# Kernel tuning notes

Measured on AMD Instinct MI355X. Metric: run time of the kernel, lower is better.

The kernel has to match this reference:

```python
import jax, jax.numpy as jnp
import numpy as np

B, D, FD, HW, NH, NC = 8, 384, 256, 64, 8, 4
NP = HW * HW
HD = D // NH


def _ln(x, g, b, eps=1e-5):
    m = jnp.mean(x, -1, keepdims=True)
    v = jnp.mean((x - m) ** 2, -1, keepdims=True)
    return (x - m) / jnp.sqrt(v + eps) * g + b


def _grn(x, g, b, eps=1e-6):
    # x: [B, D, H, W]; global L2 norm per channel over spatial dims
    gx = jnp.sqrt(jnp.sum(x * x, axis=(-2, -1), keepdims=True))  # [B,D,1,1]
    nx = gx / (jnp.mean(gx, axis=-3, keepdims=True) + eps)
    return (1.0 + g[:, None, None]) * (x * nx) + b[:, None, None] + x


def _adaln(x, film, W, bW, g, b):
    gb = film @ W.T + bW                       # [B, 2D]
    gamma, beta = jnp.split(gb, 2, axis=-1)
    return _grn(x, g, b) * (1.0 + gamma)[:, :, None, None] + beta[:, :, None, None]


def setup_inputs() -> dict:
    ks = jax.random.split(jax.random.key(0), 24)
    n = lambda k, s: jax.random.normal(k, s, jnp.float32)
    w = lambda k, o, i: n(k, (o, i)) * 0.02
    return {
        "image": n(ks[0], (B, D, HW, HW)),
        "film_vector": n(ks[1], (B, FD)),
        "perm": jax.random.permutation(ks[2], NP).astype(jnp.int32),
        "Wq": w(ks[3], D, D), "bq": jnp.zeros(D),
        "Wk": w(ks[4], D, D), "bk": jnp.zeros(D),
        "Wv": w(ks[5], D, D), "bv": jnp.zeros(D),
        "Wo": w(ks[6], D, D), "bo": jnp.zeros(D),
        "lnq_g": jnp.ones(D), "lnq_b": jnp.zeros(D),
        "lnk_g": jnp.ones(D), "lnk_b": jnp.zeros(D),
        "ada1_W": n(ks[7], (2 * D, FD)) * 0.001, "ada1_b": jnp.zeros(2 * D),
        "grn1_g": jnp.zeros(D), "grn1_b": jnp.zeros(D),
        "ada2_W": n(ks[8], (2 * D, FD)) * 0.001, "ada2_b": jnp.zeros(2 * D),
        "grn2_g": jnp.zeros(D), "grn2_b": jnp.zeros(D),
        "conv1_W": w(ks[9], 4 * D, D), "conv1_b": jnp.zeros(4 * D),
        "conv2_W": w(ks[10], D, 4 * D), "conv2_b": jnp.zeros(D),
        "cloud_scalar": jnp.ones(D),
        "ffn_scalar": jnp.ones(D),
        "final_scalar": jnp.ones(D) * 0.1,
        "num_clouds": NC,
    }


def reference(image, film_vector, perm, Wq, bq, Wk, bk, Wv, bv, Wo, bo,
              lnq_g, lnq_b, lnk_g, lnk_b, ada1_W, ada1_b, grn1_g, grn1_b,
              ada2_W, ada2_b, grn2_g, grn2_b, conv1_W, conv1_b, conv2_W, conv2_b,
              cloud_scalar, ffn_scalar, final_scalar, num_clouds):
    b, d, h, w = image.shape
    tp = h * w
    gs = tp // num_clouds

    # ---- cloud attention branch ----
    x = _adaln(image, film_vector, ada1_W, ada1_b, grn1_g, grn1_b)
    x_sh = x.reshape(b, d, tp)[:, :, perm]                       # shuffled pixels
    xg = x_sh.transpose(0, 2, 1).reshape(b * num_clouds, gs, d)  # [b*nc, gs, d]

    q = _ln(xg @ Wq.T + bq, lnq_g, lnq_b)
    k = _ln(xg @ Wk.T + bk, lnk_g, lnk_b)
    v = (xg @ Wv.T + bv).reshape(-1, gs, NH, HD)
    q = jax.nn.elu(q.reshape(-1, gs, NH, HD)) + 1.0
    k = jax.nn.elu(k.reshape(-1, gs, NH, HD)) + 1.0

    kv = jnp.einsum('bnhd,bnhe->bhde', k, v)                 # [b*nc, H, hd, hd]
    ksum = k.sum(axis=1)                                      # [b*nc, H, hd]
    num = jnp.einsum('bqhd,bhde->bqhe', q, kv)
    den = jnp.einsum('bqhd,bhd->bqh', q, ksum)[..., None] + 1e-8
    ao = (num / den).reshape(-1, gs, d) @ Wo.T + bo           # [b*nc, gs, d]

    ao = ao.reshape(b, num_clouds, gs, d).transpose(0, 3, 1, 2).reshape(b, d, tp)
    inv_perm = jnp.argsort(perm)
    ao = ao[:, :, inv_perm].reshape(b, d, h, w)

    wi = image + ao * cloud_scalar[:, None, None]

    # ---- FFN branch (1x1 convs) ----
    x2 = _adaln(wi, film_vector, ada2_W, ada2_b, grn2_g, grn2_b)
    h1 = jax.nn.silu(jnp.einsum('bdhw,ed->behw', x2, conv1_W) + conv1_b[:, None, None])
    fo = jnp.einsum('behw,de->bdhw', h1, conv2_W) + conv2_b[:, None, None]
    wi = wi + fo * ffn_scalar[:, None, None]

    return image + wi * final_scalar[:, None, None]
```

## Files before the change

kernel.cpp:

```cpp
#include <hip/hip_runtime.h>
#include <hip/hip_bf16.h>
#include <math.h>

#define BB      8
#define DD      384
#define FDIM    256
#define NPIX    4096
#define NHEAD   8
#define NCLOUD  4
#define HDIM    48
#define GSZ     1024
#define TT      (BB*NPIX)
#define DHID    (4*DD)
#define TD      1152

typedef __hip_bfloat16 bf16;
typedef __attribute__((ext_vector_type(8))) short bf16x8;
typedef __attribute__((ext_vector_type(4))) float f32x4;

__device__ __forceinline__ float b2f(bf16 x){ return __bfloat162float(x); }
__device__ __forceinline__ bf16  f2b(float x){ return __float2bfloat16(x); }
__device__ __forceinline__ float lo2f(unsigned u){ union{unsigned i; float f;} c; c.i = u << 16; return c.f; }
__device__ __forceinline__ float hi2f(unsigned u){ union{unsigned i; float f;} c; c.i = u & 0xffff0000u; return c.f; }
__device__ __forceinline__ unsigned short f2bs(float x){ bf16 b = f2b(x); return *(unsigned short*)&b; }
__device__ __forceinline__ unsigned pack2(float a, float b){
    return (unsigned)f2bs(a) | ((unsigned)f2bs(b) << 16);
}

#if defined(__has_builtin)
#if __has_builtin(__builtin_amdgcn_global_load_lds)
#define USE_GLL 1
#endif
#endif
#ifndef USE_GLL
#define USE_GLL 0
#endif

typedef __attribute__((address_space(1))) void gas_t;
typedef __attribute__((address_space(3))) void las_t;
__device__ __forceinline__ void gload16(const void* g, void* l){
#if USE_GLL
    __builtin_amdgcn_global_load_lds((gas_t*)(void*)g, (las_t*)l, 16, 0, 0);
#else
    *(bf16x8*)l = *(const bf16x8*)g;
#endif
}

__device__ __forceinline__ float block_sum(float v, float* sm, int nthreads){
    #pragma unroll
    for (int o = 32; o > 0; o >>= 1) v += __shfl_down(v, o, 64);
    int nw = nthreads >> 6;
    __syncthreads();
    if ((threadIdx.x & 63) == 0) sm[threadIdx.x >> 6] = v;
    __syncthreads();
    float s = sm[0];
    for (int i = 1; i < nw; i++) s += sm[i];
    return s;
}

#define WSEG 147456
#define WBIG 589824
__global__ void prologue(const float* Wq, const float* Wk, const float* Wv, const float* Wo,
                         const float* W1, const float* W2, bf16* wb,
                         const float* film, const float* ada1_W, const float* ada1_b,
                         const float* ada2_W, const float* ada2_b, float* gb1, float* gb2,
                         const int* perm, int* invp,
                         const float* bq, const float* bk, const float* bv, float* bqkv,
                         float* gxsq, float* gxsq2){
    int blk = blockIdx.x, tid = threadIdx.x;
    if (blk < 6912){
        int i = blk*256 + tid;
        float v;
        if      (i <   WSEG) v = Wq[i];
        else if (i < 2*WSEG) v = Wk[i -   WSEG];
        else if (i < 3*WSEG) v = Wv[i - 2*WSEG];
        else if (i < 4*WSEG) v = Wo[i - 3*WSEG];
        else if (i < 4*WSEG + WBIG) v = W1[i - 4*WSEG];
        else v = W2[i - 4*WSEG - WBIG];
        wb[i] = f2b(v);
    } else if (blk < 6960){
        int idx = (blk-6912)*256 + tid;
        int which = idx / (BB*768);
        int r = idx % (BB*768);
        int bb = r / 768, j = r % 768;
        const float* W = which ? ada2_W : ada1_W;
        const float* bi = which ? ada2_b : ada1_b;
        const float* f = film + bb*FDIM;
        const float* w = W + (size_t)j*FDIM;
        float s = 0.f;
        for (int i = 0; i < FDIM; i++) s += f[i]*w[i];
        (which ? gb2 : gb1)[bb*768 + j] = s + bi[j];
    } else if (blk < 6976){
        int i = (blk-6960)*256 + tid;
        if (i < NPIX) invp[perm[i]] = i;
    } else if (blk < 6981){
        int i = (blk-6976)*256 + tid;
        if (i < 384) bqkv[i] = bq[i];
        else if (i < 768) bqkv[i] = bk[i-384];
        else if (i < 1152) bqkv[i] = bv[i-768];
    } else {
        int i = (blk-6981)*256 + tid;
        if (i < BB*DD){ gxsq[i] = 0.f; gxsq2[i] = 0.f; }
    }
}

__global__ void prep1(const float* img, bf16* imgT, float* gxsq){
    __shared__ float tile[32][33];
    __shared__ float red[32][8];
    int b = blockIdx.z, p0 = blockIdx.x*32, d0 = blockIdx.y*32;
    int tx = threadIdx.x, ty = threadIdx.y;
    #pragma unroll
    for (int i = 0; i < 32; i += 8)
        tile[ty+i][tx] = img[((size_t)b*DD + d0+ty+i)*NPIX + p0+tx];
    __syncthreads();
    #pragma unroll
    for (int i = 0; i < 32; i += 8){
        int p = p0 + ty + i;
        imgT[((size_t)(b<<12) + p)*DD + d0+tx] = f2b(tile[tx][ty+i]);
    }
    float s = 0.f;
    #pragma unroll
    for (int k = 0; k < 4; k++){ float v = tile[tx][ty*4 + k]; s += v*v; }
    red[tx][ty] = s;
    __syncthreads();
    if (ty == 0){
        float t2 = 0.f;
        #pragma unroll
        for (int k = 0; k < 8; k++) t2 += red[tx][k];
        atomicAdd(&gxsq[b*DD + d0+tx], t2);
    }
}

template<bool SQ>
__global__ void grn_nx(const float* gin, float* nx){
    __shared__ float sm[6];
    int b = blockIdx.x; int d = threadIdx.x;
    float g = gin[b*DD + d];
    if (SQ) g = sqrtf(g);
    float tot = block_sum(g, sm, 384);
    nx[b*DD + d] = g / (tot/(float)DD + 1e-6f);
}

__global__ __launch_bounds__(256) void adaln1_tok(const bf16* imgT, const float* nx,
                        const float* gg, const float* gbv, const float* gb,
                        const int* invp, bf16* xt){
    int t = blockIdx.x*4 + (threadIdx.x >> 6);
    int lane = threadIdx.x & 63;
    int b = t >> 12, p = t & 4095;
    int j = invp[p];
    const unsigned* src = (const unsigned*)(imgT + (size_t)t*DD);
    unsigned* dst = (unsigned*)(xt + ((size_t)(b<<12) + j)*DD);
    int d0 = lane*6;
    const float* nxp = nx + b*DD + d0;
    const float* g1 = gb + b*768 + d0;
    const float* g2 = gb + b*768 + 384 + d0;
    #pragma unroll
    for (int i = 0; i < 3; i++){
        unsigned u = src[lane*3 + i];
        float v0 = lo2f(u), v1 = hi2f(u);
        int dd0 = 2*i, dd1 = 2*i+1;
        float r0 = ((1.f + gg[d0+dd0])*(v0*nxp[dd0]) + gbv[d0+dd0] + v0)*(1.f + g1[dd0]) + g2[dd0];
        float r1 = ((1.f + gg[d0+dd1])*(v1*nxp[dd1]) + gbv[d0+dd1] + v1)*(1.f + g1[dd1]) + g2[dd1];
        dst[lane*3 + i] = pack2(r0, r1);
    }
}

__global__ __launch_bounds__(256) void adaln2_tok(const bf16* wi, const float* nx,
                        const float* gg, const float* gbv, const float* gb, bf16* xout){
    int t = blockIdx.x*4 + (threadIdx.x >> 6);
    int lane = threadIdx.x & 63;
    int b = t >> 12;
    const unsigned* src = (const unsigned*)(wi + (size_t)t*DD);
    unsigned* dst = (unsigned*)(xout + (size_t)t*DD);
    int d0 = lane*6;
    const float* nxp = nx + b*DD + d0;
    const float* g1 = gb + b*768 + d0;
    const float* g2 = gb + b*768 + 384 + d0;
    #pragma unroll
    for (int i = 0; i < 3; i++){
        unsigned u = src[lane*3 + i];
        float v0 = lo2f(u), v1 = hi2f(u);
        int dd0 = 2*i, dd1 = 2*i+1;
        float r0 = ((1.f + gg[d0+dd0])*(v0*nxp[dd0]) + gbv[d0+dd0] + v0)*(1.f + g1[dd0]) + g2[dd0];
        float r1 = ((1.f + gg[d0+dd1])*(v1*nxp[dd1]) + gbv[d0+dd1] + v1)*(1.f + g1[dd1]) + g2[dd1];
        dst[lane*3 + i] = pack2(r0, r1);
    }
}

template<int EPI>
__global__ __launch_bounds__(256) void gemm_mfma(const bf16* __restrict__ A,
                          const bf16* __restrict__ W,
                          const float* __restrict__ bias,
                          bf16* __restrict__ C,
                          int M, int N, int K, const int* __restrict__ rowmap){
    __shared__ short lds_[8192];
    int tid  = threadIdx.x;
    int lane = tid & 63, wid = tid >> 6;
    int quad = lane >> 4, l16 = lane & 15;
    int wm = (wid >> 1) * 64, wn = (wid & 1) * 64;

    int v = blockIdx.y * gridDim.x + blockIdx.x;
    int xcd = v & 7, ii = v >> 3;
    int by = xcd * 32 + ii / gridDim.x;
    int bx = ii % gridDim.x;
    int m0 = by * 128, n0 = bx * 128;

    const bf16* sp[4]; short* lp[4];
    #pragma unroll
    for (int it = 0; it < 4; it++){
        int s = tid + it*256;
        int half = s >> 9;
        int r = (s >> 2) & 127;
        int seg = s & 3;
        sp[it] = (half ? W + (size_t)(n0 + r)*K : A + (size_t)(m0 + r)*K) + seg*8;
        lp[it] = lds_ + (size_t)s*8;
    }

    f32x4 acc[4][4] = {};
    for (int k0 = 0; k0 < K; k0 += 32){
        #pragma unroll
        for (int it = 0; it < 4; it++) gload16(sp[it] + k0, lp[it]);
        __syncthreads();
        bf16x8 af[4], wf[4];
        #pragma unroll
        for (int t = 0; t < 4; t++){
            af[t] = *(const bf16x8*)(void*)(lds_ + (wm + t*16 + l16)*32 + quad*8);
            wf[t] = *(const bf16x8*)(void*)(lds_ + 4096 + (wn + t*16 + l16)*32 + quad*8);
        }
        #pragma unroll
        for (int i = 0; i < 4; i++)
            #pragma unroll
            for (int j2 = 0; j2 < 4; j2++)
                acc[i][j2] = __builtin_amdgcn_mfma_f32_16x16x32_bf16(af[i], wf[j2], acc[i][j2], 0, 0, 0);
        __syncthreads();
    }
    int colbase = n0 + wn + l16;
    float bs[4];
    #pragma unroll
    for (int j2 = 0; j2 < 4; j2++) bs[j2] = bias[colbase + j2*16];
    #pragma unroll
    for (int i = 0; i < 4; i++){
        #pragma unroll
        for (int r = 0; r < 4; r++){
            int row = m0 + wm + i*16 + quad*4 + r;
            int grow = rowmap ? ((row & ~4095) | rowmap[row & 4095]) : row;
            bf16* cp = C + (size_t)grow*N + colbase;
            #pragma unroll
            for (int j2 = 0; j2 < 4; j2++){
                float vv = acc[i][j2][r] + bs[j2];
                if (EPI == 1) vv = vv / (1.f + __expf(-vv));
                cp[j2*16] = f2b(vv);
            }
        }
    }
}

__global__ __launch_bounds__(256) void ln_elu_qk(bf16* qkv,
                        const float* gq, const float* bq2,
                        const float* gk, const float* bk2){
    int r = blockIdx.x*4 + (threadIdx.x >> 6);
    int lane = threadIdx.x & 63;
    int t = r >> 1, which = r & 1;
    unsigned* row32 = (unsigned*)(qkv + (size_t)t*TD + which*384);
    const float* g = which ? gk : gq;
    const float* b = which ? bk2 : bq2;
    unsigned u[3];
    #pragma unroll
    for (int i = 0; i < 3; i++) u[i] = row32[lane*3 + i];
    float vv[6];
    #pragma unroll
    for (int i = 0; i < 3; i++){ vv[2*i] = lo2f(u[i]); vv[2*i+1] = hi2f(u[i]); }
    float s = 0.f;
    #pragma unroll
    for (int i = 0; i < 6; i++) s += vv[i];
    #pragma unroll
    for (int o = 32; o > 0; o >>= 1) s += __shfl_xor(s, o, 64);
    float mean = s / (float)DD;
    float s2 = 0.f;
    #pragma unroll
    for (int i = 0; i < 6; i++){ float d = vv[i]-mean; s2 += d*d; }
    #pragma unroll
    for (int o = 32; o > 0; o >>= 1) s2 += __shfl_xor(s2, o, 64);
    float rstd = rsqrtf(s2/(float)DD + 1e-5f);
    int d0 = lane*6;
    #pragma unroll
    for (int i = 0; i < 3; i++){
        float y0 = (vv[2*i]-mean)*rstd*g[d0+2*i] + b[d0+2*i];
        float y1 = (vv[2*i+1]-mean)*rstd*g[d0+2*i+1] + b[d0+2*i+1];
        y0 = (y0 > 0.f) ? y0 : expm1f(y0);
        y1 = (y1 > 0.f) ? y1 : expm1f(y1);
        row32[lane*3 + i] = pack2(y0 + 1.f, y1 + 1.f);
    }
}

__global__ __launch_bounds__(256) void kv_ksum_part(const bf16* qkv, float* kvp, float* ksp){
    int bch = blockIdx.x >> 3, sub = blockIdx.x & 7;
    int bc = bch >> 3, h = bch & 7;
    __shared__ float ks[16][49];
    __shared__ float vs[16][49];
    int eg = (threadIdx.x >> 4) * 3;
    int fg = (threadIdx.x & 15) * 3;
    float acc[3][3] = {};
    float ksacc[3] = {};
    int nbase = bc*GSZ + sub*128;
    for (int n0 = 0; n0 < 128; n0 += 16){
        for (int i = threadIdx.x; i < 16*48; i += 256){
            int n = i/48, e = i%48;
            size_t base = (size_t)(nbase + n0 + n)*TD + h*HDIM;
            ks[n][e] = b2f(qkv[base + 384 + e]);
            vs[n][e] = b2f(qkv[base + 768 + e]);
        }
        __syncthreads();
        #pragma unroll 4
        for (int n = 0; n < 16; n++){
            float ka[3], vb[3];
            #pragma unroll
            for (int i = 0; i < 3; i++){ ka[i] = ks[n][eg+i]; vb[i] = vs[n][fg+i]; }
            #pragma unroll
            for (int i = 0; i < 3; i++)
                #pragma unroll
                for (int j = 0; j < 3; j++)
                    acc[i][j] += ka[i]*vb[j];
            if ((threadIdx.x & 15) == 0){
                #pragma unroll
                for (int i = 0; i < 3; i++) ksacc[i] += ka[i];
            }
        }
        __syncthreads();
    }
    float* kvo = kvp + (size_t)blockIdx.x*2304;
    #pragma unroll
    for (int i = 0; i < 3; i++)
        #pragma unroll
        for (int j = 0; j < 3; j++)
            kvo[(eg+i)*48 + fg+j] = acc[i][j];
    if ((threadIdx.x & 15) == 0){
        #pragma unroll
        for (int i = 0; i < 3; i++) ksp[(size_t)blockIdx.x*48 + eg+i] = ksacc[i];
    }
}

__global__ void kv_reduce(const float* kvp, const float* ksp, float* kv, float* ksum){
    int idx = blockIdx.x*256 + threadIdx.x;
    if (idx < 256*2304){
        int bch = idx / 2304, r = idx - bch*2304;
        const float* p = kvp + (size_t)bch*8*2304 + r;
        float s = 0.f;
        #pragma unroll
        for (int u = 0; u < 8; u++) s += p[u*2304];
        kv[idx] = s;
    } else if (idx < 256*2304 + 256*48){
        int k2 = idx - 256*2304;
        int bch = k2 / 48, r = k2 - bch*48;
        const float* p = ksp + (size_t)bch*8*48 + r;
        float s = 0.f;
        #pragma unroll
        for (int u = 0; u < 8; u++) s += p[u*48];
        ksum[k2] = s;
    }
}

__global__ __launch_bounds__(256) void attn_apply(const bf16* __restrict__ qkv,
                                                  const float* __restrict__ kv,
                                                  const float* __restrict__ ksum,
                                                  bf16* __restrict__ out){
    __shared__ __align__(16) bf16 Wm[64][72];
    int bch = blockIdx.x >> 2, rs = blockIdx.x & 3;
    int bc = bch >> 3, h = bch & 7;
    int tid = threadIdx.x;
    int lane = tid & 63, w = tid >> 6;
    int l16 = lane & 15, quad = lane >> 4;

    for (int i = tid; i < 64*72; i += 256) ((unsigned short*)Wm)[i] = 0;
    __syncthreads();
    const float* kvh = kv + (size_t)bch*(HDIM*HDIM);
    for (int i = tid; i < HDIM*HDIM; i += 256){
        int e = i / HDIM, f = i - e*HDIM;
        Wm[f][e] = f2b(kvh[i]);
    }
    if (tid < HDIM) Wm[HDIM][tid] = f2b(ksum[(size_t)bch*HDIM + tid]);
    __syncthreads();

    bf16x8 bw[4][2];
    #pragma unroll
    for (int n = 0; n < 4; n++){
        bw[n][0] = *(const bf16x8*)(void*)&Wm[n*16 + l16][quad*8];
        bw[n][1] = *(const bf16x8*)(void*)&Wm[n*16 + l16][32 + quad*8];
    }

    int rowbase0 = bc*GSZ + rs*256 + w*64;
    #pragma unroll
    for (int frag = 0; frag < 4; frag++){
        int arow = rowbase0 + frag*16 + l16;
        const bf16* qp = qkv + (size_t)arow*TD + h*HDIM;
        bf16x8 a0 = *(const bf16x8*)(void*)(qp + quad*8);
        bf16x8 a1 = {};
        if (quad < 2) a1 = *(const bf16x8*)(void*)(qp + 32 + quad*8);
        f32x4 acc[4] = {};
        #pragma unroll
        for (int n = 0; n < 4; n++){
            acc[n] = __builtin_amdgcn_mfma_f32_16x16x32_bf16(a0, bw[n][0], acc[n], 0, 0, 0);
            acc[n] = __builtin_amdgcn_mfma_f32_16x16x32_bf16(a1, bw[n][1], acc[n], 0, 0, 0);
        }
        int orow0 = rowbase0 + frag*16 + quad*4;
        #pragma unroll
        for (int r = 0; r < 4; r++){
            float den = __shfl(acc[3][r], quad*16, 64);
            float inv = 1.f / (den + 1e-8f);
            bf16* op = out + (size_t)(orow0 + r)*DD + h*HDIM + l16;
            op[0]  = f2b(acc[0][r]*inv);
            op[16] = f2b(acc[1][r]*inv);
            op[32] = f2b(acc[2][r]*inv);
        }
    }
}

__global__ __launch_bounds__(256) void build_wi_colsq(const bf16* imgT, const bf16* aot,
                        const float* cs, bf16* wi, float* gxsq2){
    __shared__ float red[4][DD];
    int wave = threadIdx.x >> 6, lane = threadIdx.x & 63;
    int t0 = blockIdx.x*128 + wave*32;
    int b = (blockIdx.x*128) >> 12;
    int d0 = lane*6;
    float c[6];
    #pragma unroll
    for (int i = 0; i < 6; i++) c[i] = cs[d0+i];
    float acc[6] = {};
    for (int it = 0; it < 32; it++){
        size_t t = (size_t)(t0 + it);
        const unsigned* pi = (const unsigned*)(imgT + t*DD);
        const unsigned* pa = (const unsigned*)(aot + t*DD);
        unsigned* pw = (unsigned*)(wi + t*DD);
        #pragma unroll
        for (int i = 0; i < 3; i++){
            unsigned ui = pi[lane*3 + i];
            unsigned ua = pa[lane*3 + i];
            float v0 = lo2f(ui) + lo2f(ua)*c[2*i];
            float v1 = hi2f(ui) + hi2f(ua)*c[2*i+1];
            acc[2*i]   += v0*v0;
            acc[2*i+1] += v1*v1;
            pw[lane*3 + i] = pack2(v0, v1);
        }
    }
    #pragma unroll
    for (int i = 0; i < 6; i++) red[wave][d0+i] = acc[i];
    __syncthreads();
    for (int d = threadIdx.x; d < DD; d += 256){
        float s = red[0][d] + red[1][d] + red[2][d] + red[3][d];
        atomicAdd(&gxsq2[b*DD + d], s);
    }
}

__global__ void final_out(const float* img, const bf16* wi, const bf16* fot,
                          const float* ffs, const float* fins, float* out){
    __shared__ float tile[32][33];
    int b = blockIdx.z, p0 = blockIdx.x*32, d0 = blockIdx.y*32;
    int tx = threadIdx.x, ty = threadIdx.y;
    #pragma unroll
    for (int i = 0; i < 32; i += 8){
        size_t t = (size_t)(b<<12) + p0+ty+i;
        tile[ty+i][tx] = b2f(wi[t*DD + d0+tx]) + b2f(fot[t*DD + d0+tx])*ffs[d0+tx];
    }
    __syncthreads();
    #pragma unroll
    for (int i = 0; i < 32; i += 8){
        int d = d0 + ty + i;
        size_t o = ((size_t)b*DD + d)*NPIX + p0+tx;
        out[o] = img[o] + tile[tx][ty+i]*fins[d];
    }
}

extern "C" void kernel_launch(void* const* d_in, const int* in_sizes, int n_in,
                              void* d_out, int out_size, void* d_ws, size_t ws_size,
                              hipStream_t stream){
    const float* image   = (const float*)d_in[0];
    const float* film    = (const float*)d_in[1];
    const int*   perm    = (const int*)  d_in[2];
    const float* Wq      = (const float*)d_in[3];
    const float* bq      = (const float*)d_in[4];
    const float* Wk      = (const float*)d_in[5];
    const float* bk      = (const float*)d_in[6];
    const float* Wv      = (const float*)d_in[7];
    const float* bv      = (const float*)d_in[8];
    const float* Wo      = (const float*)d_in[9];
    const float* bo      = (const float*)d_in[10];
    const float* lnq_g   = (const float*)d_in[11];
    const float* lnq_b   = (const float*)d_in[12];
    const float* lnk_g   = (const float*)d_in[13];
    const float* lnk_b   = (const float*)d_in[14];
    const float* ada1_W  = (const float*)d_in[15];
    const float* ada1_b  = (const float*)d_in[16];
    const float* grn1_g  = (const float*)d_in[17];
    const float* grn1_b  = (const float*)d_in[18];
    const float* ada2_W  = (const float*)d_in[19];
    const float* ada2_b  = (const float*)d_in[20];
    const float* grn2_g  = (const float*)d_in[21];
    const float* grn2_b  = (const float*)d_in[22];
    const float* conv1_W = (const float*)d_in[23];
    const float* conv1_b = (const float*)d_in[24];
    const float* conv2_W = (const float*)d_in[25];
    const float* conv2_b = (const float*)d_in[26];
    const float* cs      = (const float*)d_in[27];
    const float* ffs     = (const float*)d_in[28];
    const float* fins    = (const float*)d_in[29];
    float* out = (float*)d_out;

    char* m = (char*)d_ws;
    float* gb1     = (float*)m;  m += (size_t)BB*768*4;
    float* gb2     = (float*)m;  m += (size_t)BB*768*4;
    int*   invp    = (int*)m;    m += (size_t)NPIX*4;
    float* gxsq    = (float*)m;  m += (size_t)BB*DD*4;
    float* gxsq2   = (float*)m;  m += (size_t)BB*DD*4;
    float* nx      = (float*)m;  m += (size_t)BB*DD*4;
    float* kvbuf   = (float*)m;  m += (size_t)256*HDIM*HDIM*4;
    float* ksumbuf = (float*)m;  m += (size_t)256*HDIM*4;
    float* kvp     = (float*)m;  m += (size_t)2048*2304*4;
    float* ksp     = (float*)m;  m += (size_t)2048*48*4;
    float* bqkv    = (float*)m;  m += (size_t)TD*4;
    bf16*  wb      = (bf16*)m;   m += (size_t)(4*WSEG + 2*WBIG)*2;
    bf16*  wqkv = wb;
    bf16*  wbo  = wb + 3*WSEG;
    bf16*  wb1  = wb + 4*WSEG, *wb2 = wb + 4*WSEG + WBIG;
    bf16* imgT = (bf16*)m;       m += (size_t)TT*DD*2;
    bf16* qkv = (bf16*)m;        m += (size_t)TT*TD*2;
    bf16* obf = (bf16*)m;        m += (size_t)TT*DD*2;
    bf16* abf = (bf16*)m;        m += (size_t)TT*DD*2;
    bf16* wi  = (bf16*)m;        m += (size_t)TT*DD*2;
    bf16* H1  = qkv;

    prologue<<<6993, 256, 0, stream>>>(Wq, Wk, Wv, Wo, conv1_W, conv2_W, wb,
                                       film, ada1_W, ada1_b, ada2_W, ada2_b, gb1, gb2,
                                       perm, invp, bq, bk, bv, bqkv, gxsq, gxsq2);

    prep1<<<dim3(128,12,BB), dim3(32,8), 0, stream>>>(image, imgT, gxsq);
    grn_nx<true><<<BB, DD, 0, stream>>>(gxsq, nx);
    adaln1_tok<<<TT/4, 256, 0, stream>>>(imgT, nx, grn1_g, grn1_b, gb1, invp, abf);
    gemm_mfma<0><<<dim3(9,256), 256, 0, stream>>>(abf, wqkv, bqkv, qkv, TT, TD, DD, nullptr);
    ln_elu_qk<<<2*TT/4, 256, 0, stream>>>(qkv, lnq_g, lnq_b, lnk_g, lnk_b);
    kv_ksum_part<<<2048, 256, 0, stream>>>(qkv, kvp, ksp);
    kv_reduce<<<2352, 256, 0, stream>>>(kvp, ksp, kvbuf, ksumbuf);
    attn_apply<<<1024, 256, 0, stream>>>(qkv, kvbuf, ksumbuf, abf);
    gemm_mfma<0><<<dim3(3,256), 256, 0, stream>>>(abf, wbo, bo, obf, TT, DD, DD, perm);
    build_wi_colsq<<<BB*32, 256, 0, stream>>>(imgT, obf, cs, wi, gxsq2);

    grn_nx<true><<<BB, DD, 0, stream>>>(gxsq2, nx);
    adaln2_tok<<<TT/4, 256, 0, stream>>>(wi, nx, grn2_g, grn2_b, gb2, abf);
    gemm_mfma<1><<<dim3(12,256), 256, 0, stream>>>(abf, wb1, conv1_b, H1, TT, DHID, DD, nullptr);
    gemm_mfma<0><<<dim3(3,256), 256, 0, stream>>>(H1, wb2, conv2_b, abf, TT, DD, DHID, nullptr);
    final_out<<<dim3(128,12,BB), dim3(32,8), 0, stream>>>(image, wi, abf, ffs, fins, out);
}
```

Baseline: 548.2 us.

## Fuse residual add into output-projection GEMM epilogue and transpose MFMA output layout

The MFMA operands are swapped so each lane holds four consecutive output columns. The epilogue can then store 8-byte packed bf16 vectors instead of scattered 2-byte writes. The Wo projection GEMM gets a new epilogue mode that adds the image residual times cloud_scalar and writes wi directly. The build_wi kernel shrinks to a column sum-of-squares pass over wi. This removes one full intermediate tensor write and read, at the cost of an extra imgT gather inside the GEMM epilogue.

```diff
diff --git a/kernel.cpp b/kernel.cpp
--- a/kernel.cpp
+++ b/kernel.cpp
@@ -17,6 +17,7 @@
 typedef __hip_bfloat16 bf16;
 typedef __attribute__((ext_vector_type(8))) short bf16x8;
 typedef __attribute__((ext_vector_type(4))) float f32x4;
+typedef __attribute__((ext_vector_type(2))) unsigned int u32x2;
 
 __device__ __forceinline__ float b2f(bf16 x){ return __bfloat162float(x); }
 __device__ __forceinline__ bf16  f2b(float x){ return __float2bfloat16(x); }
@@ -192,7 +193,8 @@
                           const bf16* __restrict__ W,
                           const float* __restrict__ bias,
                           bf16* __restrict__ C,
-                          int M, int N, int K, const int* __restrict__ rowmap){
+                          int M, int N, int K, const int* __restrict__ rowmap,
+                          const bf16* __restrict__ imgT, const float* __restrict__ csc){
     __shared__ short lds_[8192];
     int tid  = threadIdx.x;
     int lane = tid & 63, wid = tid >> 6;
@@ -231,26 +233,46 @@
         for (int i = 0; i < 4; i++)
             #pragma unroll
             for (int j2 = 0; j2 < 4; j2++)
-                acc[i][j2] = __builtin_amdgcn_mfma_f32_16x16x32_bf16(af[i], wf[j2], acc[i][j2], 0, 0, 0);
+                acc[i][j2] = __builtin_amdgcn_mfma_f32_16x16x32_bf16(wf[j2], af[i], acc[i][j2], 0, 0, 0);
         __syncthreads();
     }
-    int colbase = n0 + wn + l16;
-    float bs[4];
-    #pragma unroll
-    for (int j2 = 0; j2 < 4; j2++) bs[j2] = bias[colbase + j2*16];
+    int nbase = n0 + wn + quad*4;
+    f32x4 bsv[4], csv[4];
+    #pragma unroll
+    for (int j2 = 0; j2 < 4; j2++) bsv[j2] = *(const f32x4*)(bias + nbase + j2*16);
+    if (EPI == 2){
+        #pragma unroll
+        for (int j2 = 0; j2 < 4; j2++) csv[j2] = *(const f32x4*)(csc + nbase + j2*16);
+    }
     #pragma unroll
     for (int i = 0; i < 4; i++){
-        #pragma unroll
-        for (int r = 0; r < 4; r++){
-            int row = m0 + wm + i*16 + quad*4 + r;
-            int grow = rowmap ? ((row & ~4095) | rowmap[row & 4095]) : row;
-            bf16* cp = C + (size_t)grow*N + colbase;
-            #pragma unroll
-            for (int j2 = 0; j2 < 4; j2++){
-                float vv = acc[i][j2][r] + bs[j2];
-                if (EPI == 1) vv = vv / (1.f + __expf(-vv));
-                cp[j2*16] = f2b(vv);
+        int row = m0 + wm + i*16 + l16;
+        int grow = rowmap ? ((row & ~4095) | rowmap[row & 4095]) : row;
+        bf16* cp = C + (size_t)grow*N + nbase;
+        const bf16* ip = imgT + (size_t)grow*DD + nbase;
+        #pragma unroll
+        for (int j2 = 0; j2 < 4; j2++){
+            float v0 = acc[i][j2][0] + bsv[j2][0];
+            float v1 = acc[i][j2][1] + bsv[j2][1];
+            float v2 = acc[i][j2][2] + bsv[j2][2];
+            float v3 = acc[i][j2][3] + bsv[j2][3];
+            if (EPI == 1){
+                v0 = v0 / (1.f + __expf(-v0));
+                v1 = v1 / (1.f + __expf(-v1));
+                v2 = v2 / (1.f + __expf(-v2));
+                v3 = v3 / (1.f + __expf(-v3));
             }
+            if (EPI == 2){
+                u32x2 iw = *(const u32x2*)(void*)(ip + j2*16);
+                v0 = lo2f(iw.x) + v0*csv[j2][0];
+                v1 = hi2f(iw.x) + v1*csv[j2][1];
+                v2 = lo2f(iw.y) + v2*csv[j2][2];
+                v3 = hi2f(iw.y) + v3*csv[j2][3];
+            }
+            u32x2 st;
+            st.x = pack2(v0, v1);
+            st.y = pack2(v2, v3);
+            *(u32x2*)(void*)(cp + j2*16) = st;
         }
     }
 }
@@ -415,31 +437,21 @@
     }
 }
 
-__global__ __launch_bounds__(256) void build_wi_colsq(const bf16* imgT, const bf16* aot,
-                        const float* cs, bf16* wi, float* gxsq2){
+__global__ __launch_bounds__(256) void colsq(const bf16* wi, float* gxsq2){
     __shared__ float red[4][DD];
     int wave = threadIdx.x >> 6, lane = threadIdx.x & 63;
     int t0 = blockIdx.x*128 + wave*32;
     int b = (blockIdx.x*128) >> 12;
     int d0 = lane*6;
-    float c[6];
-    #pragma unroll
-    for (int i = 0; i < 6; i++) c[i] = cs[d0+i];
     float acc[6] = {};
     for (int it = 0; it < 32; it++){
-        size_t t = (size_t)(t0 + it);
-        const unsigned* pi = (const unsigned*)(imgT + t*DD);
-        const unsigned* pa = (const unsigned*)(aot + t*DD);
-        unsigned* pw = (unsigned*)(wi + t*DD);
+        const unsigned* pw = (const unsigned*)(wi + (size_t)(t0 + it)*DD);
         #pragma unroll
         for (int i = 0; i < 3; i++){
-            unsigned ui = pi[lane*3 + i];
-            unsigned ua = pa[lane*3 + i];
-            float v0 = lo2f(ui) + lo2f(ua)*c[2*i];
-            float v1 = hi2f(ui) + hi2f(ua)*c[2*i+1];
+            unsigned u = pw[lane*3 + i];
+            float v0 = lo2f(u), v1 = hi2f(u);
             acc[2*i]   += v0*v0;
             acc[2*i+1] += v1*v1;
-            pw[lane*3 + i] = pack2(v0, v1);
         }
     }
     #pragma unroll
@@ -527,6 +539,7 @@
     bf16* abf = (bf16*)m;        m += (size_t)TT*DD*2;
     bf16* wi  = (bf16*)m;        m += (size_t)TT*DD*2;
     bf16* H1  = qkv;
+    (void)obf;
 
     prologue<<<6993, 256, 0, stream>>>(Wq, Wk, Wv, Wo, conv1_W, conv2_W, wb,
                                        film, ada1_W, ada1_b, ada2_W, ada2_b, gb1, gb2,
@@ -535,17 +548,17 @@
     prep1<<<dim3(128,12,BB), dim3(32,8), 0, stream>>>(image, imgT, gxsq);
     grn_nx<true><<<BB, DD, 0, stream>>>(gxsq, nx);
     adaln1_tok<<<TT/4, 256, 0, stream>>>(imgT, nx, grn1_g, grn1_b, gb1, invp, abf);
-    gemm_mfma<0><<<dim3(9,256), 256, 0, stream>>>(abf, wqkv, bqkv, qkv, TT, TD, DD, nullptr);
+    gemm_mfma<0><<<dim3(9,256), 256, 0, stream>>>(abf, wqkv, bqkv, qkv, TT, TD, DD, nullptr, nullptr, nullptr);
     ln_elu_qk<<<2*TT/4, 256, 0, stream>>>(qkv, lnq_g, lnq_b, lnk_g, lnk_b);
     kv_ksum_part<<<2048, 256, 0, stream>>>(qkv, kvp, ksp);
     kv_reduce<<<2352, 256, 0, stream>>>(kvp, ksp, kvbuf, ksumbuf);
     attn_apply<<<1024, 256, 0, stream>>>(qkv, kvbuf, ksumbuf, abf);
-    gemm_mfma<0><<<dim3(3,256), 256, 0, stream>>>(abf, wbo, bo, obf, TT, DD, DD, perm);
-    build_wi_colsq<<<BB*32, 256, 0, stream>>>(imgT, obf, cs, wi, gxsq2);
+    gemm_mfma<2><<<dim3(3,256), 256, 0, stream>>>(abf, wbo, bo, wi, TT, DD, DD, perm, imgT, cs);
+    colsq<<<BB*32, 256, 0, stream>>>(wi, gxsq2);
 
     grn_nx<true><<<BB, DD, 0, stream>>>(gxsq2, nx);
     adaln2_tok<<<TT/4, 256, 0, stream>>>(wi, nx, grn2_g, grn2_b, gb2, abf);
-    gemm_mfma<1><<<dim3(12,256), 256, 0, stream>>>(abf, wb1, conv1_b, H1, TT, DHID, DD, nullptr);
-    gemm_mfma<0><<<dim3(3,256), 256, 0, stream>>>(H1, wb2, conv2_b, abf, TT, DD, DHID, nullptr);
+    gemm_mfma<1><<<dim3(12,256), 256, 0, stream>>>(abf, wb1, conv1_b, H1, TT, DHID, DD, nullptr, nullptr, nullptr);
+    gemm_mfma<0><<<dim3(3,256), 256, 0, stream>>>(H1, wb2, conv2_b, abf, TT, DD, DHID, nullptr, nullptr, nullptr);
     final_out<<<dim3(128,12,BB), dim3(32,8), 0, stream>>>(image, wi, abf, ffs, fins, out);
 }
```

Result: no change. 556.3 us (+1.5%).
